# Performance work log

Measured on AMD Instinct MI355X. Metric: run time of the kernel, lower is better.

## Reference

```python
import jax, jax.numpy as jnp
import numpy as np

IMG = 224   # img_size
K = 8       # num_bands
E = 256     # embed_dim


def _radial_masks(size, k):
    # Faithful to torch _create_radial_masks: center = size//2, max_r = size/sqrt(2)
    center = size // 2
    y, x = jnp.meshgrid(jnp.arange(size), jnp.arange(size), indexing='ij')
    r = jnp.sqrt(((x - center) ** 2 + (y - center) ** 2).astype(jnp.float32))
    max_r = size / np.sqrt(2.0)
    step = np.float32(max_r / k)
    i = jnp.arange(k, dtype=jnp.float32)[:, None, None]
    masks = ((r[None] >= step * i) & (r[None] < step * (i + 1.0))).astype(jnp.float32)
    return masks  # [K, H, W]


def setup_inputs() -> dict:
    key = jax.random.key(0)
    ks = jax.random.split(key, 3)
    x = jax.random.normal(ks[0], (64, 3, IMG, IMG), dtype=jnp.float32)
    W1 = jax.random.normal(ks[1], (3, E), dtype=jnp.float32) * 0.3
    b1 = jnp.zeros((E,), jnp.float32)
    gamma = jnp.ones((E,), jnp.float32)
    beta = jnp.zeros((E,), jnp.float32)
    W2 = jax.random.normal(ks[2], (E, E), dtype=jnp.float32) * (1.0 / np.sqrt(E))
    b2 = jnp.zeros((E,), jnp.float32)
    return {"x": x, "W1": W1, "b1": b1, "gamma": gamma, "beta": beta, "W2": W2, "b2": b2}


def reference(x, W1, b1, gamma, beta, W2, b2):
    masks = _radial_masks(IMG, K)                    # [K,H,W], binary, non-overlapping
    x_gray = x.mean(axis=1)                          # [B,H,W]
    fft = jnp.fft.fftshift(jnp.fft.fft2(x_gray), axes=(-2, -1))
    mag = jnp.log1p(jnp.abs(fft))                    # log(1+|F|)
    mu = mag.mean(axis=(1, 2), keepdims=True)
    sd = jnp.std(mag, axis=(1, 2), keepdims=True, ddof=1) + 1e-6  # torch .std is unbiased
    magn = (mag - mu) / sd                           # [B,H,W]

    msum = masks.sum(axis=(1, 2))                    # [K], true mask pixel counts
    mask_sums = msum + 1e-6
    s1 = jnp.einsum('bhw,khw->bk', magn, masks)      # per-band sum
    s2 = jnp.einsum('bhw,khw->bk', magn * magn, masks)
    means = s1 / mask_sums
    # sum((magn - means)^2 * mask) = s2 - 2*means*s1 + means^2 * msum  (exact expansion)
    var_num = s2 - 2.0 * means * s1 + (means ** 2) * msum
    stds = jnp.sqrt(var_num / mask_sums + 1e-6)
    # masked_fill(mask==0, -1e9) then amax over H,W
    maxs = jnp.max(jnp.where(masks[None] > 0, magn[:, None], -1e9), axis=(2, 3))

    feats = jnp.stack([means, stds, maxs], axis=-1)  # [B,K,3]
    h = feats @ W1 + b1                              # [B,K,E]
    hm = h.mean(axis=-1, keepdims=True)
    hv = h.var(axis=-1, keepdims=True)
    h = (h - hm) / jnp.sqrt(hv + 1e-5) * gamma + beta  # LayerNorm, eps=1e-5
    h = jax.nn.relu(h)
    return h @ W2 + b2                               # [B,K,E]
```

## Files before the change

### kernel.cpp

```cpp
#include <hip/hip_runtime.h>
#include <math.h>

#define IMG 224
#define NPIX 50176
#define BATCH 64
#define EDIM 256

typedef _Float16 f16;
typedef __attribute__((ext_vector_type(8))) _Float16 f16x8;
typedef __attribute__((ext_vector_type(4))) _Float16 f16x4;
typedef __attribute__((ext_vector_type(4))) float f32x4;
typedef unsigned int u32;


#define GLD16(gp, lp)                                                          \
  __builtin_amdgcn_global_load_lds(                                            \
      (const __attribute__((address_space(1))) u32*)(gp),                      \
      (__attribute__((address_space(3))) u32*)(lp), 16, 0, 0)

__global__ __launch_bounds__(256) void gemmA_kernel(const float* __restrict__ x,
                                                    f16* __restrict__ B2t,
                                                    float* __restrict__ stats) {
  __shared__ float T[224];
  __shared__ f16 As[2][32][64];
  __shared__ f16 Bs[2][256][64];
  int m0 = blockIdx.x * 32;
  int tid = threadIdx.x;
  int lane = tid & 63, wid = tid >> 6;

  if (blockIdx.x == 0) {
#pragma unroll
    for (int i = 0; i < 9; ++i) {
      int idx = i * 256 + tid;
      if (idx < BATCH * 34) stats[idx] = 0.f;
    }
  }

  int arow = tid >> 3;
  int aseg = tid & 7;
  int am = m0 + arow;
  int ab = am / 224, ah = am - ab * 224;
  const float* px = x + (size_t)ab * 3 * NPIX + ah * IMG;
  int s0 = aseg ^ (arow & 7);

  f32x4 xl[3][2];
  f32x4 acc[2][4];
#pragma unroll
  for (int i = 0; i < 2; ++i)
#pragma unroll
    for (int j = 0; j < 4; ++j) acc[i][j] = (f32x4){0.f, 0.f, 0.f, 0.f};

  auto issueA = [&](int t) {
    int kb = t * 64 + aseg * 8;
    if (kb < 224) {
#pragma unroll
      for (int c = 0; c < 3; ++c) {
        xl[c][0] = *(const f32x4*)(px + c * NPIX + kb);
        xl[c][1] = *(const f32x4*)(px + c * NPIX + kb + 4);
      }
    }
  };
  auto writeA = [&](int bufi, int t) {
    int kb = t * 64 + aseg * 8;
    f16x8 h0;
    if (kb < 224) {
#pragma unroll
      for (int j = 0; j < 8; ++j) {
        int q = j >> 2, r = j & 3;
        h0[j] = (f16)((xl[0][q][r] + xl[1][q][r] + xl[2][q][r]) * (1.0f / 3.0f));
      }
    } else {
#pragma unroll
      for (int j = 0; j < 8; ++j) h0[j] = (f16)0.f;
    }
    *(f16x8*)&As[bufi][arow][s0 * 8] = h0;
  };
  auto computeB = [&](int bufi, int t) {
    int row = tid;
    int v = (row < 113) ? row : row - 113;
    u32 off = (row < 113) ? 0u : 56u;
    u32 idx0 = ((u32)(t * 64) * (u32)v + off) % 224u;
    u32 idxm = (idx0 >= (u32)v) ? idx0 - (u32)v : idx0 + 224u - (u32)v;
    float cur = T[idx0];
    float prev = T[idxm];
    float k2c = 2.0f * T[v];
#pragma unroll
    for (int g = 0; g < 8; ++g) {
      f16x8 hv;
#pragma unroll
      for (int j = 0; j < 8; ++j) {
        hv[j] = (f16)cur;
        float nxt = __builtin_fmaf(k2c, cur, -prev);
        prev = cur; cur = nxt;
      }
      *(f16x8*)&Bs[bufi][row][(g ^ (row & 7)) * 8] = hv;
    }
  };

  issueA(0);
  if (tid < 224) T[tid] = cospif((float)tid / 112.0f);
  __syncthreads();
  computeB(0, 0);

#pragma unroll 1
  for (int t = 0; t < 4; ++t) {
    int cur = t & 1;
    asm volatile("s_waitcnt vmcnt(0)" ::: "memory");
    writeA(cur, t);
    asm volatile("s_waitcnt lgkmcnt(0)" ::: "memory");
    __builtin_amdgcn_s_barrier();
    if (t < 3) { issueA(t + 1); computeB(cur ^ 1, t + 1); }
#pragma unroll
    for (int kk = 0; kk < 2; ++kk) {
      f16x8 af[2], bfr[4];
#pragma unroll
      for (int mi = 0; mi < 2; ++mi) {
        int row = mi * 16 + (lane & 15);
        int slot = (kk * 4 + (lane >> 4)) ^ (row & 7);
        af[mi] = *(const f16x8*)&As[cur][row][slot * 8];
      }
#pragma unroll
      for (int nj = 0; nj < 4; ++nj) {
        int row = wid * 64 + nj * 16 + (lane & 15);
        int slot = (kk * 4 + (lane >> 4)) ^ (row & 7);
        bfr[nj] = *(const f16x8*)&Bs[cur][row][slot * 8];
      }
#pragma unroll
      for (int mi = 0; mi < 2; ++mi)
#pragma unroll
        for (int nj = 0; nj < 4; ++nj)
          acc[mi][nj] = __builtin_amdgcn_mfma_f32_16x16x32_f16(
              af[mi], bfr[nj], acc[mi][nj], 0, 0, 0);
    }
    __builtin_amdgcn_s_barrier();
  }

  int nbase = wid * 64;
#pragma unroll
  for (int mi = 0; mi < 2; ++mi) {
#pragma unroll
    for (int nj = 0; nj < 4; ++nj) {
      int c = nbase + nj * 16 + (lane & 15);
      if (c >= 226) continue;
      int m = m0 + mi * 16 + ((lane >> 4) << 2);
      int b = m / 224;
      int h = m - b * 224;
      int v = c, kb = h;
      if (c >= 113) { v = c - 113; kb = 224 + h; }
      size_t off = (size_t)(b * 128 + v) * 448 + kb;
      f32x4 y = acc[mi][nj];
      f16x4 hv;
#pragma unroll
      for (int r = 0; r < 4; ++r) hv[r] = (f16)y[r];
      *(f16x4*)&B2t[off] = hv;
    }
  }
}

__global__ __launch_bounds__(256) void gemmB_kernel(const f16* __restrict__ B2t,
                                                    float* __restrict__ stats) {
  __shared__ float T[224];
  __shared__ f16 As[2][64][64];
  __shared__ f16 Bs[3][128][64];
  int tid = threadIdx.x;
  int lane = tid & 63, wid = tid >> 6;
  int wr = wid >> 1, wc = wid & 1;

  int bid = blockIdx.x;
  int nb = (bid & 7) * 56 + (bid >> 3);
  int b = nb / 7;
  int m0 = (nb - b * 7) * 64;
  const f16* Bb = B2t + (size_t)b * 128 * 448;

  int srow = lane >> 3;
  int sk8 = (lane & 7) ^ srow;

  f32x4 acc[2][4];
#pragma unroll
  for (int i = 0; i < 2; ++i)
#pragma unroll
    for (int j = 0; j < 4; ++j) acc[i][j] = (f32x4){0.f, 0.f, 0.f, 0.f};

  auto issueB = [&](int t) {
    int k0 = t * 64;
    int bi = t % 3;
#pragma unroll
    for (int ci = 0; ci < 4; ++ci) {
      int j = wid * 4 + ci;
      GLD16(Bb + (size_t)(j * 8 + srow) * 448 + k0 + sk8 * 8,
            &Bs[bi][0][0] + j * 512);
    }
  };
  auto computeA = [&](int bufi, int t) {
    int row = tid >> 2, seg = tid & 3;
    int rr = m0 + row;
    u32 u = (u32)(rr >> 1);
    int imrow = rr & 1;
    int kb = t * 64 + seg * 16;
    int kim = kb >= 224;
    u32 kq = (u32)(kb - (kim ? 224 : 0));
    u32 off = imrow ? (kim ? 0u : 56u) : (kim ? 168u : 0u);
    u32 idx0 = (u * kq + off) % 224u;
    u32 idxm = (idx0 >= u) ? idx0 - u : idx0 + 224u - u;
    float cur = T[idx0];
    float prev = T[idxm];
    float k2c = 2.0f * T[u];
#pragma unroll
    for (int g = 0; g < 2; ++g) {
      f16x8 hv;
#pragma unroll
      for (int j = 0; j < 8; ++j) {
        hv[j] = (f16)cur;
        float nxt = __builtin_fmaf(k2c, cur, -prev);
        prev = cur; cur = nxt;
      }
      *(f16x8*)&As[bufi][row][((seg * 2 + g) ^ (row & 7)) * 8] = hv;
    }
  };

  if (tid < 224) T[tid] = cospif((float)tid / 112.0f);
  issueB(0);
  issueB(1);
  __syncthreads();
  computeA(0, 0);

#pragma unroll 1
  for (int t = 0; t < 7; ++t) {
    int cur = t & 1;
    if (t < 6) {
      asm volatile("s_waitcnt vmcnt(4)" ::: "memory");
    } else {
      asm volatile("s_waitcnt vmcnt(0)" ::: "memory");
    }
    asm volatile("s_waitcnt lgkmcnt(0)" ::: "memory");
    __builtin_amdgcn_s_barrier();
    if (t + 2 <= 6) issueB(t + 2);
    if (t < 6) computeA(cur ^ 1, t + 1);
    int bcur = t % 3;
#pragma unroll
    for (int kk = 0; kk < 2; ++kk) {
      f16x8 af[2], bfr[4];
#pragma unroll
      for (int mi = 0; mi < 2; ++mi) {
        int row = wr * 32 + mi * 16 + (lane & 15);
        int slot = (kk * 4 + (lane >> 4)) ^ (row & 7);
        af[mi] = *(const f16x8*)&As[cur][row][slot * 8];
      }
#pragma unroll
      for (int nj = 0; nj < 4; ++nj) {
        int row = wc * 64 + nj * 16 + (lane & 15);
        int slot = (kk * 4 + (lane >> 4)) ^ (row & 7);
        bfr[nj] = *(const f16x8*)&Bs[bcur][row][slot * 8];
      }
#pragma unroll
      for (int mi = 0; mi < 2; ++mi)
#pragma unroll
        for (int nj = 0; nj < 4; ++nj)
          acc[mi][nj] = __builtin_amdgcn_mfma_f32_16x16x32_f16(
              af[mi], bfr[nj], acc[mi][nj], 0, 0, 0);
    }
    __builtin_amdgcn_s_barrier();
  }

  int rbase = m0 + wr * 32;
  const float step = (float)(158.39191898578665 / 8.0);
  float gsum = 0.f, gsq = 0.f;
  float s1[8] = {0}, s2[8] = {0}, cnt[8] = {0};
  float mx[8] = {0, 0, 0, 0, 0, 0, 0, 0};

#pragma unroll
  for (int mi = 0; mi < 2; ++mi) {
#pragma unroll
    for (int nj = 0; nj < 4; ++nj) {
      int n = wc * 64 + nj * 16 + (lane & 15);
      if (n >= 113) continue;
      float wgt = (n >= 1 && n <= 111) ? 2.f : 1.f;
      float dx2 = (float)(n * n);
      int rr = rbase + mi * 16 + ((lane >> 4) << 2);
      f32x4 f = acc[mi][nj];
#pragma unroll
      for (int p = 0; p < 2; ++p) {
        int u = (rr >> 1) + p;
        float re = f[2 * p], im = f[2 * p + 1];
        float mv = log1pf(sqrtf(re * re + im * im));
        int a = (u <= 111) ? u : 224 - u;
        float r = sqrtf((float)(a * a) + dx2);
        int bd = 255;
#pragma unroll
        for (int k = 0; k < 8; k++) {
          float lo = step * (float)k;
          float hi = step * (float)(k + 1);
          if (r >= lo && r < hi) bd = k;
        }
        float wm = wgt * mv;
        gsum += wm;
        gsq += wm * mv;
#pragma unroll
        for (int k = 0; k < 8; k++) {
          bool m = (bd == k);
          s1[k] += m ? wm : 0.f;
          s2[k] += m ? wm * mv : 0.f;
          cnt[k] += m ? wgt : 0.f;
          mx[k] = m ? fmaxf(mx[k], mv) : mx[k];
        }
      }
    }
  }

  float vals[34];
  vals[0] = gsum; vals[1] = gsq;
#pragma unroll
  for (int k = 0; k < 8; k++) {
    vals[2 + k] = s1[k]; vals[10 + k] = s2[k]; vals[18 + k] = mx[k]; vals[26 + k] = cnt[k];
  }
#pragma unroll
  for (int i = 0; i < 34; i++) {
    float v = vals[i];
    const bool isMax = (i >= 18 && i < 26);
#pragma unroll
    for (int off = 32; off > 0; off >>= 1) {
      float o = __shfl_down(v, off);
      v = isMax ? fmaxf(v, o) : (v + o);
    }
    vals[i] = v;
  }
  float* red = (float*)&As[0][0][0];
  if ((tid & 63) == 0) {
#pragma unroll
    for (int i = 0; i < 34; i++) red[wid * 34 + i] = vals[i];
  }
  __syncthreads();
  if (tid < 34) {
    bool isMax = (tid >= 18 && tid < 26);
    float v = red[tid];
#pragma unroll
    for (int ww = 1; ww < 4; ww++) {
      float o = red[ww * 34 + tid];
      v = isMax ? fmaxf(v, o) : (v + o);
    }
    if (isMax)
      atomicMax((u32*)&stats[b * 34 + tid], __float_as_uint(v));
    else
      atomicAdd(&stats[b * 34 + tid], v);
  }
}

__global__ __launch_bounds__(256) void mlp_kernel(const float* __restrict__ stats,
                                                  const float* __restrict__ W1,
                                                  const float* __restrict__ b1,
                                                  const float* __restrict__ gamma,
                                                  const float* __restrict__ beta,
                                                  const float* __restrict__ W2m,
                                                  const float* __restrict__ b2,
                                                  float* __restrict__ out) {
  int blk = blockIdx.x;
  int b = blk >> 2;
  int k0 = (blk & 3) * 2;
  int e = threadIdx.x;
  int lane = e & 63, wave = e >> 6;

  __shared__ float st[34];
  if (e < 34) st[e] = stats[b * 34 + e];
  __syncthreads();

  const float N = (float)NPIX;
  float mu = st[0] / N;
  float varg = fmaxf(st[1] - N * mu * mu, 0.0f) / (N - 1.0f);
  float sd = sqrtf(varg) + 1e-6f;

  float g_e = gamma[e], bt_e = beta[e], b1_e = b1[e];
  float w1a = W1[e], w1b = W1[EDIM + e], w1c = W1[2 * EDIM + e];

  float h[2];
#pragma unroll
  for (int q = 0; q < 2; ++q) {
    int k = k0 + q;
    float s1r = st[2 + k], s2r = st[10 + k], mxr = st[18 + k], cntk = st[26 + k];
    float ms = cntk + 1e-6f;
    float s1n = (s1r - mu * cntk) / sd;
    float s2n = (s2r - 2.0f * mu * s1r + mu * mu * cntk) / (sd * sd);
    float mean_k = s1n / ms;
    float var_num = s2n - 2.0f * mean_k * s1n + mean_k * mean_k * cntk;
    float std_k = sqrtf(var_num / ms + 1e-6f);
    float max_k = (mxr - mu) / sd;
    h[q] = mean_k * w1a + std_k * w1b + max_k * w1c + b1_e;
  }

  float v4[4] = {h[0], h[0] * h[0], h[1], h[1] * h[1]};
#pragma unroll
  for (int i = 0; i < 4; ++i) {
#pragma unroll
    for (int off = 32; off > 0; off >>= 1) v4[i] += __shfl_down(v4[i], off);
  }
  __shared__ float red[4][4];
  __shared__ float mm[4];
  if (lane == 0) {
#pragma unroll
    for (int i = 0; i < 4; ++i) red[wave][i] = v4[i];
  }
  __syncthreads();
  if (e == 0) {
#pragma unroll
    for (int i = 0; i < 4; ++i) {
      float t = red[0][i] + red[1][i] + red[2][i] + red[3][i];
      red[0][i] = t;
    }
    float hm0 = red[0][0] / 256.0f, hm1 = red[0][2] / 256.0f;
    mm[0] = hm0;
    mm[1] = fmaxf(red[0][1] / 256.0f - hm0 * hm0, 0.0f);
    mm[2] = hm1;
    mm[3] = fmaxf(red[0][3] / 256.0f - hm1 * hm1, 0.0f);
  }
  __syncthreads();

  __shared__ float hsT[EDIM][2];
#pragma unroll
  for (int q = 0; q < 2; ++q) {
    float hn = (h[q] - mm[2 * q]) / sqrtf(mm[2 * q + 1] + 1e-5f) * g_e + bt_e;
    hsT[e][q] = fmaxf(hn, 0.0f);
  }
  __syncthreads();

  float a0 = b2[e], a1 = a0;
#pragma unroll 8
  for (int j = 0; j < EDIM; j++) {
    float w = W2m[j * EDIM + e];
    float2 hp = *(const float2*)&hsT[j][0];
    a0 += hp.x * w;
    a1 += hp.y * w;
  }
  out[(size_t)(b * 8 + k0) * EDIM + e] = a0;
  out[(size_t)(b * 8 + k0 + 1) * EDIM + e] = a1;
}

extern "C" void kernel_launch(void* const* d_in, const int* in_sizes, int n_in,
                              void* d_out, int out_size, void* d_ws, size_t ws_size,
                              hipStream_t stream) {
  const float* x     = (const float*)d_in[0];
  const float* W1    = (const float*)d_in[1];
  const float* b1    = (const float*)d_in[2];
  const float* gamma = (const float*)d_in[3];
  const float* beta  = (const float*)d_in[4];
  const float* W2m   = (const float*)d_in[5];
  const float* b2    = (const float*)d_in[6];
  float* out = (float*)d_out;

  char* W = (char*)d_ws;
  f16* B2t = (f16*)W;
  float* stats = (float*)(W + 7340032);

  gemmA_kernel<<<dim3(448), dim3(256), 0, stream>>>(x, B2t, stats);
  gemmB_kernel<<<dim3(448), dim3(256), 0, stream>>>(B2t, stats);
  mlp_kernel<<<dim3(256), dim3(256), 0, stream>>>(stats, W1, b1, gamma, beta, W2m, b2, out);
}
```

Baseline: 49.89 us.

## Fuse MLP into last-arriving gemmB block and deepen gemmA load prefetch

Removes the separate MLP kernel launch. Each gemmB block increments a per-batch done counter, and the seventh (last) block for a batch reads the accumulated stats atomically and runs the LayerNorm+MLP for all 8 bands. gemmA is unrolled into an explicit schedule with two register buffers, so global loads for tile t+1 are issued two steps ahead with partial vmcnt waits. The risk is that the tail MLP work is serialized into 64 blocks at the end of gemmB, and the zeroed region is extended to cover the counters.

```diff
diff --git a/kernel.cpp b/kernel.cpp
--- a/kernel.cpp
+++ b/kernel.cpp
@@ -20,7 +20,7 @@
 
 __global__ __launch_bounds__(256) void gemmA_kernel(const float* __restrict__ x,
                                                     f16* __restrict__ B2t,
-                                                    float* __restrict__ stats) {
+                                                    u32* __restrict__ zero_region) {
   __shared__ float T[224];
   __shared__ f16 As[2][32][64];
   __shared__ f16 Bs[2][256][64];
@@ -32,7 +32,7 @@
 #pragma unroll
     for (int i = 0; i < 9; ++i) {
       int idx = i * 256 + tid;
-      if (idx < BATCH * 34) stats[idx] = 0.f;
+      if (idx < 2240) zero_region[idx] = 0u;
     }
   }
 
@@ -43,14 +43,14 @@
   const float* px = x + (size_t)ab * 3 * NPIX + ah * IMG;
   int s0 = aseg ^ (arow & 7);
 
-  f32x4 xl[3][2];
+  f32x4 xlA[3][2], xlB[3][2];
   f32x4 acc[2][4];
 #pragma unroll
   for (int i = 0; i < 2; ++i)
 #pragma unroll
     for (int j = 0; j < 4; ++j) acc[i][j] = (f32x4){0.f, 0.f, 0.f, 0.f};
 
-  auto issueA = [&](int t) {
+  auto issueA = [&](f32x4 (&xl)[3][2], int t) {
     int kb = t * 64 + aseg * 8;
     if (kb < 224) {
 #pragma unroll
@@ -60,7 +60,7 @@
       }
     }
   };
-  auto writeA = [&](int bufi, int t) {
+  auto writeA = [&](f32x4 (&xl)[3][2], int t, int bufi) {
     int kb = t * 64 + aseg * 8;
     f16x8 h0;
     if (kb < 224) {
@@ -96,20 +96,7 @@
       *(f16x8*)&Bs[bufi][row][(g ^ (row & 7)) * 8] = hv;
     }
   };
-
-  issueA(0);
-  if (tid < 224) T[tid] = cospif((float)tid / 112.0f);
-  __syncthreads();
-  computeB(0, 0);
-
-#pragma unroll 1
-  for (int t = 0; t < 4; ++t) {
-    int cur = t & 1;
-    asm volatile("s_waitcnt vmcnt(0)" ::: "memory");
-    writeA(cur, t);
-    asm volatile("s_waitcnt lgkmcnt(0)" ::: "memory");
-    __builtin_amdgcn_s_barrier();
-    if (t < 3) { issueA(t + 1); computeB(cur ^ 1, t + 1); }
+  auto mfmaStep = [&](int bufi) {
 #pragma unroll
     for (int kk = 0; kk < 2; ++kk) {
       f16x8 af[2], bfr[4];
@@ -117,13 +104,13 @@
       for (int mi = 0; mi < 2; ++mi) {
         int row = mi * 16 + (lane & 15);
         int slot = (kk * 4 + (lane >> 4)) ^ (row & 7);
-        af[mi] = *(const f16x8*)&As[cur][row][slot * 8];
+        af[mi] = *(const f16x8*)&As[bufi][row][slot * 8];
       }
 #pragma unroll
       for (int nj = 0; nj < 4; ++nj) {
         int row = wid * 64 + nj * 16 + (lane & 15);
         int slot = (kk * 4 + (lane >> 4)) ^ (row & 7);
-        bfr[nj] = *(const f16x8*)&Bs[cur][row][slot * 8];
+        bfr[nj] = *(const f16x8*)&Bs[bufi][row][slot * 8];
       }
 #pragma unroll
       for (int mi = 0; mi < 2; ++mi)
@@ -132,8 +119,42 @@
           acc[mi][nj] = __builtin_amdgcn_mfma_f32_16x16x32_f16(
               af[mi], bfr[nj], acc[mi][nj], 0, 0, 0);
     }
-    __builtin_amdgcn_s_barrier();
-  }
+  };
+
+  issueA(xlA, 0);
+  if (tid < 224) T[tid] = cospif((float)tid / 112.0f);
+  issueA(xlB, 1);
+  __syncthreads();
+  computeB(0, 0);
+
+  asm volatile("s_waitcnt vmcnt(6)" ::: "memory");
+  writeA(xlA, 0, 0);
+  asm volatile("s_waitcnt lgkmcnt(0)" ::: "memory");
+  __builtin_amdgcn_s_barrier();
+  issueA(xlA, 2);
+  computeB(1, 1);
+  mfmaStep(0);
+  __builtin_amdgcn_s_barrier();
+  asm volatile("s_waitcnt vmcnt(6)" ::: "memory");
+  writeA(xlB, 1, 1);
+  asm volatile("s_waitcnt lgkmcnt(0)" ::: "memory");
+  __builtin_amdgcn_s_barrier();
+  issueA(xlB, 3);
+  computeB(0, 2);
+  mfmaStep(1);
+  __builtin_amdgcn_s_barrier();
+  asm volatile("s_waitcnt vmcnt(6)" ::: "memory");
+  writeA(xlA, 2, 0);
+  asm volatile("s_waitcnt lgkmcnt(0)" ::: "memory");
+  __builtin_amdgcn_s_barrier();
+  computeB(1, 3);
+  mfmaStep(0);
+  __builtin_amdgcn_s_barrier();
+  asm volatile("s_waitcnt vmcnt(0)" ::: "memory");
+  writeA(xlB, 3, 1);
+  asm volatile("s_waitcnt lgkmcnt(0)" ::: "memory");
+  __builtin_amdgcn_s_barrier();
+  mfmaStep(1);
 
   int nbase = wid * 64;
 #pragma unroll
@@ -158,7 +179,15 @@
 }
 
 __global__ __launch_bounds__(256) void gemmB_kernel(const f16* __restrict__ B2t,
-                                                    float* __restrict__ stats) {
+                                                    float* __restrict__ stats,
+                                                    u32* __restrict__ done,
+                                                    const float* __restrict__ W1,
+                                                    const float* __restrict__ b1,
+                                                    const float* __restrict__ gamma,
+                                                    const float* __restrict__ beta,
+                                                    const float* __restrict__ W2m,
+                                                    const float* __restrict__ b2,
+                                                    float* __restrict__ out) {
   __shared__ float T[224];
   __shared__ f16 As[2][64][64];
   __shared__ f16 Bs[3][128][64];
@@ -343,26 +372,22 @@
     else
       atomicAdd(&stats[b * 34 + tid], v);
   }
-}
-
-__global__ __launch_bounds__(256) void mlp_kernel(const float* __restrict__ stats,
-                                                  const float* __restrict__ W1,
-                                                  const float* __restrict__ b1,
-                                                  const float* __restrict__ gamma,
-                                                  const float* __restrict__ beta,
-                                                  const float* __restrict__ W2m,
-                                                  const float* __restrict__ b2,
-                                                  float* __restrict__ out) {
-  int blk = blockIdx.x;
-  int b = blk >> 2;
-  int k0 = (blk & 3) * 2;
-  int e = threadIdx.x;
-  int lane = e & 63, wave = e >> 6;
+
+  __shared__ bool lastS;
+  __threadfence();
+  __syncthreads();
+  if (tid == 0) {
+    u32 old = atomicAdd(&done[b], 1u);
+    lastS = (old == 6u);
+  }
+  __syncthreads();
+  if (!lastS) return;
 
   __shared__ float st[34];
-  if (e < 34) st[e] = stats[b * 34 + e];
-  __syncthreads();
-
+  if (tid < 34) st[tid] = atomicAdd(&stats[b * 34 + tid], 0.0f);
+  __syncthreads();
+
+  int e = tid;
   const float N = (float)NPIX;
   float mu = st[0] / N;
   float varg = fmaxf(st[1] - N * mu * mu, 0.0f) / (N - 1.0f);
@@ -371,11 +396,10 @@
   float g_e = gamma[e], bt_e = beta[e], b1_e = b1[e];
   float w1a = W1[e], w1b = W1[EDIM + e], w1c = W1[2 * EDIM + e];
 
-  float h[2];
-#pragma unroll
-  for (int q = 0; q < 2; ++q) {
-    int k = k0 + q;
-    float s1r = st[2 + k], s2r = st[10 + k], mxr = st[18 + k], cntk = st[26 + k];
+  float h[8];
+#pragma unroll
+  for (int q = 0; q < 8; ++q) {
+    float s1r = st[2 + q], s2r = st[10 + q], mxr = st[18 + q], cntk = st[26 + q];
     float ms = cntk + 1e-6f;
     float s1n = (s1r - mu * cntk) / sd;
     float s2n = (s2r - 2.0f * mu * s1r + mu * mu * cntk) / (sd * sd);
@@ -386,51 +410,54 @@
     h[q] = mean_k * w1a + std_k * w1b + max_k * w1c + b1_e;
   }
 
-  float v4[4] = {h[0], h[0] * h[0], h[1], h[1] * h[1]};
-#pragma unroll
-  for (int i = 0; i < 4; ++i) {
-#pragma unroll
-    for (int off = 32; off > 0; off >>= 1) v4[i] += __shfl_down(v4[i], off);
-  }
-  __shared__ float red[4][4];
-  __shared__ float mm[4];
+  float vv[16];
+#pragma unroll
+  for (int q = 0; q < 8; ++q) { vv[2 * q] = h[q]; vv[2 * q + 1] = h[q] * h[q]; }
+#pragma unroll
+  for (int i = 0; i < 16; ++i) {
+#pragma unroll
+    for (int off = 32; off > 0; off >>= 1) vv[i] += __shfl_down(vv[i], off);
+  }
+  __shared__ float red2[4][16];
   if (lane == 0) {
 #pragma unroll
-    for (int i = 0; i < 4; ++i) red[wave][i] = v4[i];
-  }
-  __syncthreads();
-  if (e == 0) {
-#pragma unroll
-    for (int i = 0; i < 4; ++i) {
-      float t = red[0][i] + red[1][i] + red[2][i] + red[3][i];
-      red[0][i] = t;
-    }
-    float hm0 = red[0][0] / 256.0f, hm1 = red[0][2] / 256.0f;
-    mm[0] = hm0;
-    mm[1] = fmaxf(red[0][1] / 256.0f - hm0 * hm0, 0.0f);
-    mm[2] = hm1;
-    mm[3] = fmaxf(red[0][3] / 256.0f - hm1 * hm1, 0.0f);
-  }
-  __syncthreads();
-
-  __shared__ float hsT[EDIM][2];
-#pragma unroll
-  for (int q = 0; q < 2; ++q) {
-    float hn = (h[q] - mm[2 * q]) / sqrtf(mm[2 * q + 1] + 1e-5f) * g_e + bt_e;
+    for (int i = 0; i < 16; ++i) red2[wid][i] = vv[i];
+  }
+  __syncthreads();
+  __shared__ float mm2[16];
+  if (tid < 8) {
+    float s = 0.f, qq = 0.f;
+#pragma unroll
+    for (int w = 0; w < 4; ++w) { s += red2[w][2 * tid]; qq += red2[w][2 * tid + 1]; }
+    float hm = s / 256.0f;
+    mm2[2 * tid] = hm;
+    mm2[2 * tid + 1] = fmaxf(qq / 256.0f - hm * hm, 0.0f);
+  }
+  __syncthreads();
+
+  float (*hsT)[8] = (float(*)[8]) & As[0][0][0];
+#pragma unroll
+  for (int q = 0; q < 8; ++q) {
+    float hn = (h[q] - mm2[2 * q]) / sqrtf(mm2[2 * q + 1] + 1e-5f) * g_e + bt_e;
     hsT[e][q] = fmaxf(hn, 0.0f);
   }
   __syncthreads();
 
-  float a0 = b2[e], a1 = a0;
+  float a[8];
+  float b2e = b2[e];
+#pragma unroll
+  for (int q = 0; q < 8; ++q) a[q] = b2e;
 #pragma unroll 8
-  for (int j = 0; j < EDIM; j++) {
+  for (int j = 0; j < EDIM; ++j) {
     float w = W2m[j * EDIM + e];
-    float2 hp = *(const float2*)&hsT[j][0];
-    a0 += hp.x * w;
-    a1 += hp.y * w;
-  }
-  out[(size_t)(b * 8 + k0) * EDIM + e] = a0;
-  out[(size_t)(b * 8 + k0 + 1) * EDIM + e] = a1;
+    f32x4 p0 = *(const f32x4*)&hsT[j][0];
+    f32x4 p1 = *(const f32x4*)&hsT[j][4];
+    a[0] += p0[0] * w; a[1] += p0[1] * w; a[2] += p0[2] * w; a[3] += p0[3] * w;
+    a[4] += p1[0] * w; a[5] += p1[1] * w; a[6] += p1[2] * w; a[7] += p1[3] * w;
+  }
+#pragma unroll
+  for (int q = 0; q < 8; ++q)
+    out[(size_t)(b * 8 + q) * EDIM + e] = a[q];
 }
 
 extern "C" void kernel_launch(void* const* d_in, const int* in_sizes, int n_in,
@@ -448,8 +475,9 @@
   char* W = (char*)d_ws;
   f16* B2t = (f16*)W;
   float* stats = (float*)(W + 7340032);
-
-  gemmA_kernel<<<dim3(448), dim3(256), 0, stream>>>(x, B2t, stats);
-  gemmB_kernel<<<dim3(448), dim3(256), 0, stream>>>(B2t, stats);
-  mlp_kernel<<<dim3(256), dim3(256), 0, stream>>>(stats, W1, b1, gamma, beta, W2m, b2, out);
+  u32* done = (u32*)(W + 7340032 + 8704);
+
+  gemmA_kernel<<<dim3(448), dim3(256), 0, stream>>>(x, B2t, (u32*)stats);
+  gemmB_kernel<<<dim3(448), dim3(256), 0, stream>>>(B2t, stats, done,
+                                                    W1, b1, gamma, beta, W2m, b2, out);
 }
```

Result: slower. 74.65 us (+49.6%).

## Precompute DFT twiddle matrix in gemmA and stream it via async loads in gemmB

Applied to the files above, without the earlier changes.

gemmA now double-buffers its global x loads in registers and unrolls the four K-steps so the next tile's loads overlap the current MFMA step. It also writes the full 448x448 fp16 cos/sin twiddle matrix to workspace, one row per block. gemmB no longer generates its A operand with a Chebyshev recurrence in LDS. It loads that operand from the precomputed matrix with global_load_lds, alongside B, in a two-stage pipeline. The launch grid changes to (batch, 7) and the block-swizzled index mapping is dropped, so gemmB reads more from global and L2 and may lose L2 locality.

```diff
diff --git a/kernel.cpp b/kernel.cpp
--- a/kernel.cpp
+++ b/kernel.cpp
@@ -20,7 +20,8 @@
 
 __global__ __launch_bounds__(256) void gemmA_kernel(const float* __restrict__ x,
                                                     f16* __restrict__ B2t,
-                                                    float* __restrict__ stats) {
+                                                    f16* __restrict__ W2h,
+                                                    u32* __restrict__ statsz) {
   __shared__ float T[224];
   __shared__ f16 As[2][32][64];
   __shared__ f16 Bs[2][256][64];
@@ -32,7 +33,7 @@
 #pragma unroll
     for (int i = 0; i < 9; ++i) {
       int idx = i * 256 + tid;
-      if (idx < BATCH * 34) stats[idx] = 0.f;
+      if (idx < 2176) statsz[idx] = 0u;
     }
   }
 
@@ -43,14 +44,14 @@
   const float* px = x + (size_t)ab * 3 * NPIX + ah * IMG;
   int s0 = aseg ^ (arow & 7);
 
-  f32x4 xl[3][2];
+  f32x4 xlA[3][2], xlB[3][2];
   f32x4 acc[2][4];
 #pragma unroll
   for (int i = 0; i < 2; ++i)
 #pragma unroll
     for (int j = 0; j < 4; ++j) acc[i][j] = (f32x4){0.f, 0.f, 0.f, 0.f};
 
-  auto issueA = [&](int t) {
+  auto issueA = [&](f32x4 (&xl)[3][2], int t) {
     int kb = t * 64 + aseg * 8;
     if (kb < 224) {
 #pragma unroll
@@ -60,7 +61,7 @@
       }
     }
   };
-  auto writeA = [&](int bufi, int t) {
+  auto writeA = [&](f32x4 (&xl)[3][2], int t, int bufi) {
     int kb = t * 64 + aseg * 8;
     f16x8 h0;
     if (kb < 224) {
@@ -96,20 +97,7 @@
       *(f16x8*)&Bs[bufi][row][(g ^ (row & 7)) * 8] = hv;
     }
   };
-
-  issueA(0);
-  if (tid < 224) T[tid] = cospif((float)tid / 112.0f);
-  __syncthreads();
-  computeB(0, 0);
-
-#pragma unroll 1
-  for (int t = 0; t < 4; ++t) {
-    int cur = t & 1;
-    asm volatile("s_waitcnt vmcnt(0)" ::: "memory");
-    writeA(cur, t);
-    asm volatile("s_waitcnt lgkmcnt(0)" ::: "memory");
-    __builtin_amdgcn_s_barrier();
-    if (t < 3) { issueA(t + 1); computeB(cur ^ 1, t + 1); }
+  auto mfmaStep = [&](int bufi) {
 #pragma unroll
     for (int kk = 0; kk < 2; ++kk) {
       f16x8 af[2], bfr[4];
@@ -117,13 +105,13 @@
       for (int mi = 0; mi < 2; ++mi) {
         int row = mi * 16 + (lane & 15);
         int slot = (kk * 4 + (lane >> 4)) ^ (row & 7);
-        af[mi] = *(const f16x8*)&As[cur][row][slot * 8];
+        af[mi] = *(const f16x8*)&As[bufi][row][slot * 8];
       }
 #pragma unroll
       for (int nj = 0; nj < 4; ++nj) {
         int row = wid * 64 + nj * 16 + (lane & 15);
         int slot = (kk * 4 + (lane >> 4)) ^ (row & 7);
-        bfr[nj] = *(const f16x8*)&Bs[cur][row][slot * 8];
+        bfr[nj] = *(const f16x8*)&Bs[bufi][row][slot * 8];
       }
 #pragma unroll
       for (int mi = 0; mi < 2; ++mi)
@@ -132,8 +120,42 @@
           acc[mi][nj] = __builtin_amdgcn_mfma_f32_16x16x32_f16(
               af[mi], bfr[nj], acc[mi][nj], 0, 0, 0);
     }
-    __builtin_amdgcn_s_barrier();
-  }
+  };
+
+  issueA(xlA, 0);
+  if (tid < 224) T[tid] = cospif((float)tid / 112.0f);
+  issueA(xlB, 1);
+  __syncthreads();
+  computeB(0, 0);
+
+  asm volatile("s_waitcnt vmcnt(6)" ::: "memory");
+  writeA(xlA, 0, 0);
+  asm volatile("s_waitcnt lgkmcnt(0)" ::: "memory");
+  __builtin_amdgcn_s_barrier();
+  issueA(xlA, 2);
+  computeB(1, 1);
+  mfmaStep(0);
+  __builtin_amdgcn_s_barrier();
+  asm volatile("s_waitcnt vmcnt(6)" ::: "memory");
+  writeA(xlB, 1, 1);
+  asm volatile("s_waitcnt lgkmcnt(0)" ::: "memory");
+  __builtin_amdgcn_s_barrier();
+  issueA(xlB, 3);
+  computeB(0, 2);
+  mfmaStep(1);
+  __builtin_amdgcn_s_barrier();
+  asm volatile("s_waitcnt vmcnt(6)" ::: "memory");
+  writeA(xlA, 2, 0);
+  asm volatile("s_waitcnt lgkmcnt(0)" ::: "memory");
+  __builtin_amdgcn_s_barrier();
+  computeB(1, 3);
+  mfmaStep(0);
+  __builtin_amdgcn_s_barrier();
+  asm volatile("s_waitcnt vmcnt(0)" ::: "memory");
+  writeA(xlB, 3, 1);
+  asm volatile("s_waitcnt lgkmcnt(0)" ::: "memory");
+  __builtin_amdgcn_s_barrier();
+  mfmaStep(1);
 
   int nbase = wid * 64;
 #pragma unroll
@@ -155,22 +177,39 @@
       *(f16x4*)&B2t[off] = hv;
     }
   }
+
+  {
+    int r = blockIdx.x;
+    int u = r >> 1;
+    bool imrow = r & 1;
+#pragma unroll
+    for (int pass = 0; pass < 2; ++pass) {
+      int k = pass * 256 + tid;
+      if (k < 448) {
+        bool kim = k >= 224;
+        int kk = kim ? k - 224 : k;
+        int m = (u * kk) % 224;
+        float mf = (float)m / 112.0f;
+        float c = cospif(mf), s = sinpif(mf);
+        float val = imrow ? (kim ? c : -s) : (kim ? s : c);
+        W2h[(size_t)r * 448 + k] = (f16)val;
+      }
+    }
+  }
 }
 
-__global__ __launch_bounds__(256) void gemmB_kernel(const f16* __restrict__ B2t,
+__global__ __launch_bounds__(256) void gemmB_kernel(const f16* __restrict__ W2h,
+                                                    const f16* __restrict__ B2t,
                                                     float* __restrict__ stats) {
-  __shared__ float T[224];
   __shared__ f16 As[2][64][64];
-  __shared__ f16 Bs[3][128][64];
+  __shared__ f16 Bs[2][128][64];
+  int b = blockIdx.x;
+  int m0 = blockIdx.y * 64;
   int tid = threadIdx.x;
   int lane = tid & 63, wid = tid >> 6;
   int wr = wid >> 1, wc = wid & 1;
-
-  int bid = blockIdx.x;
-  int nb = (bid & 7) * 56 + (bid >> 3);
-  int b = nb / 7;
-  int m0 = (nb - b * 7) * 64;
-  const f16* Bb = B2t + (size_t)b * 128 * 448;
+  const f16* Ap = W2h + (size_t)m0 * 448;
+  const f16* Bp = B2t + (size_t)b * 128 * 448;
 
   int srow = lane >> 3;
   int sk8 = (lane & 7) ^ srow;
@@ -181,62 +220,33 @@
 #pragma unroll
     for (int j = 0; j < 4; ++j) acc[i][j] = (f32x4){0.f, 0.f, 0.f, 0.f};
 
-  auto issueB = [&](int t) {
+  auto stage = [&](int bufi, int t) {
     int k0 = t * 64;
-    int bi = t % 3;
-#pragma unroll
-    for (int ci = 0; ci < 4; ++ci) {
-      int j = wid * 4 + ci;
-      GLD16(Bb + (size_t)(j * 8 + srow) * 448 + k0 + sk8 * 8,
-            &Bs[bi][0][0] + j * 512);
+#pragma unroll
+    for (int ci = 0; ci < 6; ++ci) {
+      int c = wid * 6 + ci;
+      if (c < 8) {
+        GLD16(Ap + (size_t)(c * 8 + srow) * 448 + k0 + sk8 * 8,
+              &As[bufi][0][0] + c * 512);
+      } else {
+        int j = c - 8;
+        GLD16(Bp + (size_t)(j * 8 + srow) * 448 + k0 + sk8 * 8,
+              &Bs[bufi][0][0] + j * 512);
+      }
     }
   };
-  auto computeA = [&](int bufi, int t) {
-    int row = tid >> 2, seg = tid & 3;
-    int rr = m0 + row;
-    u32 u = (u32)(rr >> 1);
-    int imrow = rr & 1;
-    int kb = t * 64 + seg * 16;
-    int kim = kb >= 224;
-    u32 kq = (u32)(kb - (kim ? 224 : 0));
-    u32 off = imrow ? (kim ? 0u : 56u) : (kim ? 168u : 0u);
-    u32 idx0 = (u * kq + off) % 224u;
-    u32 idxm = (idx0 >= u) ? idx0 - u : idx0 + 224u - u;
-    float cur = T[idx0];
-    float prev = T[idxm];
-    float k2c = 2.0f * T[u];
-#pragma unroll
-    for (int g = 0; g < 2; ++g) {
-      f16x8 hv;
-#pragma unroll
-      for (int j = 0; j < 8; ++j) {
-        hv[j] = (f16)cur;
-        float nxt = __builtin_fmaf(k2c, cur, -prev);
-        prev = cur; cur = nxt;
-      }
-      *(f16x8*)&As[bufi][row][((seg * 2 + g) ^ (row & 7)) * 8] = hv;
-    }
-  };
-
-  if (tid < 224) T[tid] = cospif((float)tid / 112.0f);
-  issueB(0);
-  issueB(1);
-  __syncthreads();
-  computeA(0, 0);
-
+
+  stage(0, 0);
 #pragma unroll 1
   for (int t = 0; t < 7; ++t) {
     int cur = t & 1;
-    if (t < 6) {
-      asm volatile("s_waitcnt vmcnt(4)" ::: "memory");
+    if (t + 1 < 7) {
+      stage(cur ^ 1, t + 1);
+      asm volatile("s_waitcnt vmcnt(6)" ::: "memory");
     } else {
       asm volatile("s_waitcnt vmcnt(0)" ::: "memory");
     }
-    asm volatile("s_waitcnt lgkmcnt(0)" ::: "memory");
     __builtin_amdgcn_s_barrier();
-    if (t + 2 <= 6) issueB(t + 2);
-    if (t < 6) computeA(cur ^ 1, t + 1);
-    int bcur = t % 3;
 #pragma unroll
     for (int kk = 0; kk < 2; ++kk) {
       f16x8 af[2], bfr[4];
@@ -250,7 +260,7 @@
       for (int nj = 0; nj < 4; ++nj) {
         int row = wc * 64 + nj * 16 + (lane & 15);
         int slot = (kk * 4 + (lane >> 4)) ^ (row & 7);
-        bfr[nj] = *(const f16x8*)&Bs[bcur][row][slot * 8];
+        bfr[nj] = *(const f16x8*)&Bs[cur][row][slot * 8];
       }
 #pragma unroll
       for (int mi = 0; mi < 2; ++mi)
@@ -448,8 +458,9 @@
   char* W = (char*)d_ws;
   f16* B2t = (f16*)W;
   float* stats = (float*)(W + 7340032);
-
-  gemmA_kernel<<<dim3(448), dim3(256), 0, stream>>>(x, B2t, stats);
-  gemmB_kernel<<<dim3(448), dim3(256), 0, stream>>>(B2t, stats);
+  f16* W2h = (f16*)(W + 7340032 + 8704);
+
+  gemmA_kernel<<<dim3(448), dim3(256), 0, stream>>>(x, B2t, W2h, (u32*)stats);
+  gemmB_kernel<<<dim3(BATCH, 7), dim3(256), 0, stream>>>(W2h, B2t, stats);
   mlp_kernel<<<dim3(256), dim3(256), 0, stream>>>(stats, W1, b1, gamma, beta, W2m, b2, out);
 }
```

Result: no change. 50.65 us (+1.5%).
